# Performance work log

Hardware: AMD Instinct MI355X
Metric: run time of the kernel (lower is better)

The kernel has to match this reference:

```python
import jax, jax.numpy as jnp
import numpy as np

B, N, F_IN = 4, 2048, 256
K, D = 4, 64
NEG_SLOPE = 0.2


def setup_inputs() -> dict:
    key = jax.random.key(0)
    k1, k2, k3, k4, k5 = jax.random.split(key, 5)
    x = jax.random.normal(k1, (B, N, F_IN), dtype=jnp.float32)
    adj = jax.random.randint(k2, (B, N, N), 0, 2, dtype=jnp.int32)
    # xavier_uniform-style params
    def xavier(k, shape):
        fan_in, fan_out = shape[-2], shape[-1]
        lim = np.sqrt(6.0 / (fan_in + fan_out))
        return jax.random.uniform(k, shape, jnp.float32, -lim, lim)
    W = xavier(k3, (K, F_IN, D))
    a_src = xavier(k4, (K, D, 1))
    a_dst = xavier(k5, (K, D, 1))
    return {"x": x, "adj": adj, "W": W, "a_src": a_src, "a_dst": a_dst}


def reference(x, adj, W, a_src, a_dst):
    # Wh: (B, K, N, D)
    Wh = jnp.einsum('bnf,kfd->bknd', x, W)
    e_src = jnp.einsum('bknd,kdo->bkno', Wh, a_src)  # (B,K,N,1)
    e_dst = jnp.einsum('bknd,kdo->bkno', Wh, a_dst)  # (B,K,N,1)
    e = e_src + jnp.swapaxes(e_dst, -2, -1)          # (B,K,N,N)
    e = jnp.where(e > 0, e, NEG_SLOPE * e)           # LeakyReLU(0.2)
    # adjacency mask with forced self-loops (adj + I > 0)
    eye = jnp.eye(e.shape[-1], dtype=bool)
    mask = (adj[:, None, :, :] > 0) | eye            # (B,1|K,N,N)
    e = jnp.where(mask, e, -jnp.inf)
    # numerically-stable softmax matching F_module_softmax
    x_max = jnp.max(e, axis=-1, keepdims=True)
    x_max = jnp.where(jnp.isinf(x_max), 0.0, x_max)
    exp_e = jnp.exp(e - x_max)
    exp_e = jnp.where(jnp.isinf(e), 0.0, exp_e)
    alpha = exp_e / (jnp.sum(exp_e, axis=-1, keepdims=True) + 1e-10)
    # dropout is identity in eval mode
    out = jnp.matmul(alpha, Wh)                      # (B,K,N,D)
    # concat heads: (B,N,K*D)
    Bn, Kn, Nn, Dn = out.shape
    return jnp.transpose(out, (0, 2, 1, 3)).reshape(Bn, Nn, Kn * Dn)
```

## Files before the change

kernel.cpp:

```cpp
#include <hip/hip_runtime.h>

#define NB 4
#define NN 2048
#define NF 256
#define NK 4
#define ND 64
#define NEG 0.2f
#define LOG2E 1.4426950408889634f

typedef _Float16 f16;
typedef _Float16 f16x2 __attribute__((ext_vector_type(2)));
typedef _Float16 f16x4 __attribute__((ext_vector_type(4)));
typedef _Float16 f16x8 __attribute__((ext_vector_type(8)));
typedef float f32x4 __attribute__((ext_vector_type(4)));
typedef float f32x16 __attribute__((ext_vector_type(16)));
typedef unsigned int u32;
typedef unsigned short u16;

__device__ __forceinline__ int gsz(int d) { return (d ^ (d >> 3)) & 7; }

__global__ __launch_bounds__(256) void k01(
    const float* __restrict__ x,
    const int*   __restrict__ adj,
    const float* __restrict__ Wm,
    const float* __restrict__ a_src,
    const float* __restrict__ a_dst,
    unsigned int* __restrict__ abit,
    f16* __restrict__ wht,
    float* __restrict__ sbuf,
    f16* __restrict__ ebuf,
    f16* __restrict__ fbuf)
{
    __shared__ f16 wt[64 * 256];

    const int bx  = blockIdx.x;
    const int tid = threadIdx.x;

    if (bx >= 256) {
        const int row = (bx - 256) * 4 + (tid >> 6);
        const int l   = tid & 63;
        const int i   = row & (NN - 1);
        const int* __restrict__ ar = adj + (size_t)row * NN;

        int v[32];
#pragma unroll
        for (int c = 0; c < 32; ++c) v[c] = ar[c * 64 + l];

        unsigned int kx = 0, ky = 0;
#pragma unroll
        for (int c = 0; c < 32; ++c) {
            unsigned long long m = __ballot(v[c] > 0);
            if (l == c) { kx = (unsigned int)m; ky = (unsigned int)(m >> 32); }
        }
        if (l == (i >> 6)) {
            unsigned int sb = 1u << (i & 31);
            if (((i >> 5) & 1) == 0) kx |= sb; else ky |= sb;
        }
        if (l < 32) {
            uint2 kk; kk.x = kx; kk.y = ky;
            *(uint2*)&abit[(size_t)row * 64 + l * 2] = kk;
        }
        return;
    }

    const int gx  = bx & 15;
    const int k   = (bx >> 4) & 3;
    const int b   = bx >> 6;
    const int wv  = tid >> 6;
    const int l   = tid & 63;
    const int q   = l >> 4;
    const int r16 = l & 15;

    for (int fc = 0; fc < 64; ++fc) {
        int f = fc * 4 + wv;
        int d = l;
        wt[d * 256 + (f ^ ((d & 7) << 3))] = (f16)Wm[(k * NF + f) * ND + d];
    }
    __syncthreads();

    const int ncol0 = gx * 128 + wv * 32;
    f32x4 acc[2][4];
#pragma unroll
    for (int nt = 0; nt < 2; ++nt)
#pragma unroll
        for (int dt = 0; dt < 4; ++dt)
            acc[nt][dt] = (f32x4){0.f, 0.f, 0.f, 0.f};

    for (int fs = 0; fs < 16; ++fs) {
        const int f0 = fs * 16 + q * 4;
        f16x4 af[4];
#pragma unroll
        for (int dt = 0; dt < 4; ++dt) {
            int d = dt * 16 + r16;
            af[dt] = *(const f16x4*)&wt[d * 256 + (f0 ^ ((d & 7) << 3))];
        }
#pragma unroll
        for (int nt = 0; nt < 2; ++nt) {
            int n = ncol0 + nt * 16 + r16;
            float4 xv = *(const float4*)&x[((size_t)(b * NN + n)) * NF + f0];
            f16x4 bf = {(f16)xv.x, (f16)xv.y, (f16)xv.z, (f16)xv.w};
#pragma unroll
            for (int dt = 0; dt < 4; ++dt)
                acc[nt][dt] = __builtin_amdgcn_mfma_f32_16x16x16f16(
                    af[dt], bf, acc[nt][dt], 0, 0, 0);
        }
    }

    float asv[4][4], adv[4][4];
#pragma unroll
    for (int dt = 0; dt < 4; ++dt)
#pragma unroll
        for (int rr = 0; rr < 4; ++rr) {
            int d = dt * 16 + q * 4 + rr;
            asv[dt][rr] = a_src[k * ND + d];
            adv[dt][rr] = a_dst[k * ND + d];
        }

    const size_t obase = (size_t)(b * NK + k) * 131072;

#pragma unroll
    for (int nt = 0; nt < 2; ++nt) {
        int n  = ncol0 + nt * 16 + r16;
        int s_ = n >> 6, g = (n >> 3) & 7, e = n & 7;
        float sp = 0.f, tp = 0.f;
#pragma unroll
        for (int dt = 0; dt < 4; ++dt)
#pragma unroll
            for (int rr = 0; rr < 4; ++rr) {
                float v = acc[nt][dt][rr];
                int d = dt * 16 + q * 4 + rr;
                wht[obase + s_ * 4096 + d * 64 + ((g ^ gsz(d)) << 3) + e] = (f16)v;
                sp += v * asv[dt][rr];
                tp += v * adv[dt][rr];
            }
        sp += __shfl_xor(sp, 16);
        sp += __shfl_xor(sp, 32);
        tp += __shfl_xor(tp, 16);
        tp += __shfl_xor(tp, 32);
        if (q == 0) {
            int idx = (b * NK + k) * NN + n;
            sbuf[idx] = sp;
            ebuf[idx] = (f16)__builtin_exp2f(tp * LOG2E);
            fbuf[idx] = (f16)__builtin_exp2f(0.2f * LOG2E * tp);
        }
    }
}

__global__ __launch_bounds__(512, 4) void k2_attn(
    const unsigned int* __restrict__ abit,
    const f16* __restrict__ wht,
    const float* __restrict__ sbuf,
    const f16* __restrict__ ebuf,
    const f16* __restrict__ fbuf,
    float* __restrict__ out)
{
    const int bid = blockIdx.x;
    const int bkv = (bid & 7) | (((bid >> 3) & 1) << 3);
    const int rg  = bid >> 4;
    const int b   = bkv >> 2, k = bkv & 3;
    const int i0  = rg * 64;
    const int tid = threadIdx.x;
    const int w   = tid >> 6;
    const int c   = w >> 1;
    const int rw  = w & 1;
    const int l   = tid & 63;
    const int r32 = l & 31;
    const int hi  = l >> 5;
    const int iglob = i0 + rw * 32 + r32;

    __shared__ __attribute__((aligned(16))) char pool[74752];
    u16* el = (u16*)(pool + 65536);
    u16* fl = (u16*)(pool + 69632);

    const unsigned int* __restrict__ abrow =
        abit + (size_t)(b * NN + iglob) * 64 + c * 16;
    uint2 abx[8];
#pragma unroll
    for (int it = 0; it < 8; ++it) abx[it] = *(const uint2*)(abrow + it * 2);

    {
        const u16* eb = (const u16*)(ebuf + bkv * NN);
        const u16* fb = (const u16*)(fbuf + bkv * NN);
        *(ushort4*)&el[tid * 4] = *(const ushort4*)&eb[tid * 4];
        *(ushort4*)&fl[tid * 4] = *(const ushort4*)&fb[tid * 4];
    }

    const float s   = sbuf[bkv * NN + iglob];
    const f16 Afh = (f16)__builtin_exp2f(0.8f * LOG2E * fminf(s, 0.f));
    const f16 Bfh = (f16)__builtin_exp2f(-0.8f * LOG2E * fmaxf(s, 0.f));
    const f16x2 Af2 = {Afh, Afh};
    const f16x2 Bf2 = {Bfh, Bfh};
    const f16 h1 = (f16)1.0f;
    const f16x8 ones8 = {h1, h1, h1, h1, h1, h1, h1, h1};
    const char* gtiles = (const char*)wht + (size_t)bkv * 262144;

    f32x16 acc[2], accd;
#pragma unroll
    for (int z = 0; z < 16; ++z) { acc[0][z] = 0.f; acc[1][z] = 0.f; accd[z] = 0.f; }

#define STAGE8(bb, it)                                                         \
    do {                                                                       \
        const char* gsrc = gtiles + (size_t)(c * 8 + (it)) * 8192 +            \
                           rw * 1024 + l * 16;                                 \
        char* ldst = pool + c * 16384 + (bb) * 8192 + rw * 1024 + l * 16;      \
        _Pragma("unroll") for (int kk = 0; kk < 4; ++kk)                       \
            __builtin_amdgcn_global_load_lds(                                  \
                (const __attribute__((address_space(1))) void*)(gsrc +         \
                    kk * 2048),                                                \
                (__attribute__((address_space(3))) void*)(ldst + kk * 2048),   \
                16, 0, 0);                                                     \
    } while (0)

    STAGE8(0, 0);

#pragma unroll
    for (int it = 0; it < 8; ++it) {
        asm volatile("s_waitcnt vmcnt(0) lgkmcnt(0)" ::: "memory");
        __builtin_amdgcn_sched_barrier(0);
        __builtin_amdgcn_s_barrier();
        __builtin_amdgcn_sched_barrier(0);
        if (it < 7) STAGE8((it + 1) & 1, it + 1);

        const char* lb = pool + c * 16384 + (it & 1) * 8192;
        const uint2 ab = abx[it];
#pragma unroll
        for (int jts = 0; jts < 4; ++jts) {
            const u32 word = (jts & 2) ? ab.y : ab.x;
            const u32 bbyte = (word >> (((jts & 1) << 4) + (hi << 3))) & 0xffu;
            const u32 u = (bbyte << 15) | bbyte;
            const int jb = c * 512 + it * 64 + jts * 16 + hi * 8;
            uint4 E4 = *(const uint4*)&el[jb];
            uint4 F4 = *(const uint4*)&fl[jb];
            u32 pa_u[4];
#pragma unroll
            for (int p = 0; p < 4; ++p) {
                f16x2 e2 = __builtin_bit_cast(f16x2, ((const u32*)&E4)[p]);
                f16x2 f2 = __builtin_bit_cast(f16x2, ((const u32*)&F4)[p]);
                f16x2 w2 = __builtin_elementwise_max(Af2 * e2, Bf2 * f2);
                u32 x  = (u >> (2 * p)) & 0x00010001u;
                u32 mm = (x << 16) - x;
                pa_u[p] = __builtin_bit_cast(u32, w2) & mm;
            }
            uint4 pav = {pa_u[0], pa_u[1], pa_u[2], pa_u[3]};
            f16x8 pa = __builtin_bit_cast(f16x8, pav);
#pragma unroll
            for (int dh = 0; dh < 2; ++dh) {
                const int d = dh * 32 + r32;
                f16x8 v8 = *(const f16x8*)(lb + d * 128 +
                               ((((jts << 1) | hi) ^ gsz(d)) << 4));
                acc[dh] = __builtin_amdgcn_mfma_f32_32x32x16_f16(
                    pa, v8, acc[dh], 0, 0, 0);
            }
            accd = __builtin_amdgcn_mfma_f32_32x32x16_f16(pa, ones8, accd, 0, 0, 0);
        }
    }
#undef STAGE8

    __syncthreads();
    float* stash = (float*)pool;
    if (c != 0) {
        float* sb = stash + ((c - 1) * 2 + rw) * 3072 + l * 48;
#pragma unroll
        for (int dh = 0; dh < 2; ++dh)
#pragma unroll
            for (int sub = 0; sub < 4; ++sub) {
                f32x4 v = {acc[dh][sub * 4], acc[dh][sub * 4 + 1],
                           acc[dh][sub * 4 + 2], acc[dh][sub * 4 + 3]};
                *(f32x4*)&sb[dh * 16 + ((sub ^ (l & 3)) << 2)] = v;
            }
#pragma unroll
        for (int sub = 0; sub < 4; ++sub) {
            f32x4 v = {accd[sub * 4], accd[sub * 4 + 1],
                       accd[sub * 4 + 2], accd[sub * 4 + 3]};
            *(f32x4*)&sb[32 + ((sub ^ (l & 3)) << 2)] = v;
        }
    }
    __syncthreads();

    if (c == 0) {
#pragma unroll
        for (int cc = 0; cc < 3; ++cc) {
            const float* sr = stash + (cc * 2 + rw) * 3072 + l * 48;
#pragma unroll
            for (int dh = 0; dh < 2; ++dh)
#pragma unroll
                for (int sub = 0; sub < 4; ++sub) {
                    f32x4 v = *(const f32x4*)&sr[dh * 16 + ((sub ^ (l & 3)) << 2)];
#pragma unroll
                    for (int m = 0; m < 4; ++m) acc[dh][sub * 4 + m] += v[m];
                }
#pragma unroll
            for (int sub = 0; sub < 4; ++sub) {
                f32x4 v = *(const f32x4*)&sr[32 + ((sub ^ (l & 3)) << 2)];
#pragma unroll
                for (int m = 0; m < 4; ++m) accd[sub * 4 + m] += v[m];
            }
        }
        float* op = out + ((size_t)(b * NN) + i0 + rw * 32) * (NK * ND) + k * ND;
#pragma unroll
        for (int g4 = 0; g4 < 4; ++g4)
#pragma unroll
            for (int m = 0; m < 4; ++m) {
                const int rr   = g4 * 4 + m;
                const int irow = g4 * 8 + hi * 4 + m;
                const float inv = 1.f / (accd[rr] + 1e-10f);
                op[(size_t)irow * (NK * ND) + r32]      = acc[0][rr] * inv;
                op[(size_t)irow * (NK * ND) + 32 + r32] = acc[1][rr] * inv;
            }
    }
}

extern "C" void kernel_launch(void* const* d_in, const int* in_sizes, int n_in,
                              void* d_out, int out_size, void* d_ws, size_t ws_size,
                              hipStream_t stream) {
    const float* x     = (const float*)d_in[0];
    const int*   adj   = (const int*)d_in[1];
    const float* Wm    = (const float*)d_in[2];
    const float* a_src = (const float*)d_in[3];
    const float* a_dst = (const float*)d_in[4];
    float* out = (float*)d_out;

    char* ws = (char*)d_ws;
    f16*   wht  = (f16*)ws;
    float* sbuf = (float*)(ws + (4u << 20));
    f16*   ebuf = (f16*)(ws + (4u << 20) + (128u << 10));
    f16*   fbuf = (f16*)(ws + (4u << 20) + (192u << 10));
    unsigned int* abit = (unsigned int*)(ws + (4u << 20) + (256u << 10));

    k01<<<dim3(256 + NB * NN / 4), 256, 0, stream>>>(
        x, adj, Wm, a_src, a_dst, abit, wht, sbuf, ebuf, fbuf);
    k2_attn<<<dim3(512), 512, 0, stream>>>(
        abit, wht, sbuf, ebuf, fbuf, out);
}
```

Baseline: 41.99 us.

## Load Wh fragments directly from global in MFMA-ready layout, drop LDS staging

Changes the Wh output layout written by the projection kernel so that each lane's 8-element f16 fragment is contiguous in global memory. The attention kernel then reads the MFMA B operands straight from global/L2 instead of staging tiles into LDS with async global_load_lds, double buffering and per-iteration barriers. This removes the LDS traffic and the synchronisation, at the cost of exposing global load latency with no explicit prefetch pipeline, and of more scattered 16-bit stores in the producer.

New measurement: 41.64 us. About the same (-0.8%).

```diff
diff --git a/kernel.cpp b/kernel.cpp
--- a/kernel.cpp
+++ b/kernel.cpp
@@ -16,8 +16,6 @@
 typedef float f32x16 __attribute__((ext_vector_type(16)));
 typedef unsigned int u32;
 typedef unsigned short u16;
-
-__device__ __forceinline__ int gsz(int d) { return (d ^ (d >> 3)) & 7; }
 
 __global__ __launch_bounds__(256) void k01(
     const float* __restrict__ x,
@@ -121,7 +119,7 @@
 #pragma unroll
     for (int nt = 0; nt < 2; ++nt) {
         int n  = ncol0 + nt * 16 + r16;
-        int s_ = n >> 6, g = (n >> 3) & 7, e = n & 7;
+        const size_t sb_ = obase + (size_t)(n >> 3) * 512 + (n & 7);
         float sp = 0.f, tp = 0.f;
 #pragma unroll
         for (int dt = 0; dt < 4; ++dt)
@@ -129,7 +127,7 @@
             for (int rr = 0; rr < 4; ++rr) {
                 float v = acc[nt][dt][rr];
                 int d = dt * 16 + q * 4 + rr;
-                wht[obase + s_ * 4096 + d * 64 + ((g ^ gsz(d)) << 3) + e] = (f16)v;
+                wht[sb_ + d * 8] = (f16)v;
                 sp += v * asv[dt][rr];
                 tp += v * adv[dt][rr];
             }
@@ -192,36 +190,18 @@
     const f16x2 Bf2 = {Bfh, Bfh};
     const f16 h1 = (f16)1.0f;
     const f16x8 ones8 = {h1, h1, h1, h1, h1, h1, h1, h1};
-    const char* gtiles = (const char*)wht + (size_t)bkv * 262144;
+
+    const f16* __restrict__ lanep =
+        wht + (size_t)bkv * 131072 + (size_t)(c * 64 + hi) * 512 + r32 * 8;
 
     f32x16 acc[2], accd;
 #pragma unroll
     for (int z = 0; z < 16; ++z) { acc[0][z] = 0.f; acc[1][z] = 0.f; accd[z] = 0.f; }
 
-#define STAGE8(bb, it)                                                         \
-    do {                                                                       \
-        const char* gsrc = gtiles + (size_t)(c * 8 + (it)) * 8192 +            \
-                           rw * 1024 + l * 16;                                 \
-        char* ldst = pool + c * 16384 + (bb) * 8192 + rw * 1024 + l * 16;      \
-        _Pragma("unroll") for (int kk = 0; kk < 4; ++kk)                       \
-            __builtin_amdgcn_global_load_lds(                                  \
-                (const __attribute__((address_space(1))) void*)(gsrc +         \
-                    kk * 2048),                                                \
-                (__attribute__((address_space(3))) void*)(ldst + kk * 2048),   \
-                16, 0, 0);                                                     \
-    } while (0)
-
-    STAGE8(0, 0);
+    __syncthreads();
 
 #pragma unroll
     for (int it = 0; it < 8; ++it) {
-        asm volatile("s_waitcnt vmcnt(0) lgkmcnt(0)" ::: "memory");
-        __builtin_amdgcn_sched_barrier(0);
-        __builtin_amdgcn_s_barrier();
-        __builtin_amdgcn_sched_barrier(0);
-        if (it < 7) STAGE8((it + 1) & 1, it + 1);
-
-        const char* lb = pool + c * 16384 + (it & 1) * 8192;
         const uint2 ab = abx[it];
 #pragma unroll
         for (int jts = 0; jts < 4; ++jts) {
@@ -243,18 +223,15 @@
             }
             uint4 pav = {pa_u[0], pa_u[1], pa_u[2], pa_u[3]};
             f16x8 pa = __builtin_bit_cast(f16x8, pav);
-#pragma unroll
-            for (int dh = 0; dh < 2; ++dh) {
-                const int d = dh * 32 + r32;
-                f16x8 v8 = *(const f16x8*)(lb + d * 128 +
-                               ((((jts << 1) | hi) ^ gsz(d)) << 4));
-                acc[dh] = __builtin_amdgcn_mfma_f32_32x32x16_f16(
-                    pa, v8, acc[dh], 0, 0, 0);
-            }
-            accd = __builtin_amdgcn_mfma_f32_32x32x16_f16(pa, ones8, accd, 0, 0, 0);
-        }
-    }
-#undef STAGE8
+
+            const f16* fp = lanep + (size_t)(it * 8 + jts * 2) * 512;
+            f16x8 v80 = *(const f16x8*)(fp);
+            f16x8 v81 = *(const f16x8*)(fp + 256);
+            acc[0] = __builtin_amdgcn_mfma_f32_32x32x16_f16(pa, v80, acc[0], 0, 0, 0);
+            acc[1] = __builtin_amdgcn_mfma_f32_32x32x16_f16(pa, v81, acc[1], 0, 0, 0);
+            accd   = __builtin_amdgcn_mfma_f32_32x32x16_f16(pa, ones8, accd, 0, 0, 0);
+        }
+    }
 
     __syncthreads();
     float* stash = (float*)pool;
```
